# Kernel tuning notes

Measured on AMD Instinct MI355X. Metric: run time of the kernel, lower is better.

Reference implementation:

```python
import jax, jax.numpy as jnp
import numpy as np

DEFAULT_MASK_VALUE = -0.7 * float(jnp.finfo(jnp.dtype('float32')).max)

B, T, NQ, NKV, D = 2, 1024, 32, 8, 128


def setup_inputs() -> dict:
    key = jax.random.key(0)
    k1, k2, k3, k4 = jax.random.split(key, 4)
    query = jax.random.normal(k1, (B, T, NQ, D), dtype=jnp.float32)
    kk = jax.random.normal(k2, (B, T, NKV, D), dtype=jnp.float32)
    vv = jax.random.normal(k3, (B, T, NKV, D), dtype=jnp.float32)
    # packed-sequence segment ids, sorted so each segment is contiguous (values 1..3, >0 = active)
    decoder_segment_ids = jnp.sort(jax.random.randint(k4, (B, T), 1, 4), axis=-1).astype(jnp.int32)
    return {"query": query, "key": kk, "value": vv,
            "decoder_segment_ids": decoder_segment_ids}


def _attention(query, key, value, decoder_segment_ids):
    # MaxText AttentionOp.apply_attention_dot (prefill / train mode), GQA layout.
    b, t, n, d = query.shape
    n_kv = key.shape[2]
    g = n // n_kv
    q = query.reshape(b, t, n_kv, g, d)
    # qk product: [b, n_kv, g, t, s]
    logits = jnp.einsum('btkgd,bskd->bkgts', q, key)
    # generate_attention_mask: segment mask AND causal mask
    seg_mask = decoder_segment_ids[:, :, None] == decoder_segment_ids[:, None, :]  # [b,t,s]
    row_ids = jax.lax.broadcasted_iota(jnp.int32, (t, t), 0)
    col_ids = jax.lax.broadcasted_iota(jnp.int32, (t, t), 1)
    causal = col_ids <= row_ids  # [t,s]
    mask = jnp.logical_and(seg_mask, causal[None])  # [b,t,s]
    # apply_mask_to_logits: replace masked entries with DEFAULT_MASK_VALUE (avoids add fusion)
    masked = jnp.where(mask[:, None, None, :, :], logits, DEFAULT_MASK_VALUE)
    probs = jax.nn.softmax(masked, axis=-1)
    out = jnp.einsum('bkgts,bskd->btkgd', probs, value)
    return out.reshape(b, t, n, d)


def reference(query, key, value, decoder_segment_ids):
    return _attention(query, key, value, decoder_segment_ids)
```

## Files before the change

### kernel.cpp

```cpp
#include <hip/hip_runtime.h>

constexpr int B_  = 2;
constexpr int T_  = 1024;
constexpr int NQ  = 32;
constexpr int NKV = 8;
constexpr int D_  = 128;

constexpr int BM = 64;
constexpr int BN = 32;
constexpr int NTILE = T_ / BM;
constexpr float MASK_NEG = -3.0e38f;

typedef _Float16 f16;
typedef f16 f16x2 __attribute__((ext_vector_type(2)));
typedef f16 f16x4 __attribute__((ext_vector_type(4)));
typedef f16 f16x8 __attribute__((ext_vector_type(8)));
typedef float floatx4 __attribute__((ext_vector_type(4)));

__global__ __launch_bounds__(256)
void fa_kernel(const float* __restrict__ Qg, const float* __restrict__ Kg,
               const float* __restrict__ Vg, const int* __restrict__ seg,
               float* __restrict__ Og) {
    __shared__ f16 lds_k[BN][136];
    __shared__ f16 lds_vt[D_][40];
    __shared__ f16 lds_p[4][16][40];

    const int pair = blockIdx.x;
    const int h    = blockIdx.y;
    const int b    = blockIdx.z;
    const int kv   = h >> 2;

    const int tid  = threadIdx.x;
    const int wave = tid >> 6;
    const int lane = tid & 63;
    const int quad = lane >> 4;
    const int ln   = lane & 15;

    const int kd4 = tid & 31, kr8 = tid >> 5;
    const int vd  = tid & 127, vhalf = tid >> 7;

    const int* segb = seg + b * T_;

    for (int sub = 0; sub < 2; ++sub) {
        const int tile = (sub == 0) ? (NTILE - 1 - pair) : pair;
        const int t0 = tile * BM;

        const int qrow = t0 + wave * 16 + ln;
        const float* qptr = Qg + (((size_t)b * T_ + qrow) * NQ + h) * D_;
        f16x8 qfrag[4];
#pragma unroll
        for (int c = 0; c < 4; ++c) {
            const float* p = qptr + c * 32 + quad * 8;
            float4 f0 = *(const float4*)(p);
            float4 f1 = *(const float4*)(p + 4);
            f16x8 v;
            v[0] = (f16)f0.x; v[1] = (f16)f0.y; v[2] = (f16)f0.z; v[3] = (f16)f0.w;
            v[4] = (f16)f1.x; v[5] = (f16)f1.y; v[6] = (f16)f1.z; v[7] = (f16)f1.w;
            qfrag[c] = v;
        }

        int trow[4], segq[4];
#pragma unroll
        for (int r = 0; r < 4; ++r) {
            trow[r] = t0 + wave * 16 + quad * 4 + r;
            segq[r] = segb[trow[r]];
        }
        const int seg_lo = segb[t0];

        int lo = 0, hi = t0;
        while (lo < hi) {
            const int mid = (lo + hi) >> 1;
            if (segb[mid] < seg_lo) lo = mid + 1; else hi = mid;
        }
        const int blk_start = lo >> 5;
        const int nblk = 2 * tile + 2;

        float  m_i[4], l_i[4];
        floatx4 o_acc[8];
#pragma unroll
        for (int r = 0; r < 4; ++r) { m_i[r] = -1.0e30f; l_i[r] = 0.0f; }
#pragma unroll
        for (int dt = 0; dt < 8; ++dt) o_acc[dt] = floatx4{0.f, 0.f, 0.f, 0.f};

        float4 kreg[4];
        float  vreg[16];
        {
            const int s0 = blk_start * BN;
            const float* kb = Kg + (((size_t)b * T_ + s0 + kr8) * NKV + kv) * D_ + kd4 * 4;
#pragma unroll
            for (int i = 0; i < 4; ++i)
                kreg[i] = *(const float4*)(kb + (size_t)(8 * i) * NKV * D_);
            const float* vb = Vg + (((size_t)b * T_ + s0 + vhalf * 16) * NKV + kv) * D_ + vd;
#pragma unroll
            for (int i = 0; i < 16; ++i)
                vreg[i] = vb[(size_t)i * NKV * D_];
        }

        for (int blk = blk_start; blk < nblk; ++blk) {
            const int s0 = blk * BN;
            __syncthreads();

#pragma unroll
            for (int i = 0; i < 4; ++i) {
                f16x4 w;
                w[0] = (f16)kreg[i].x; w[1] = (f16)kreg[i].y;
                w[2] = (f16)kreg[i].z; w[3] = (f16)kreg[i].w;
                *(f16x4*)&lds_k[kr8 + 8 * i][kd4 * 4] = w;
            }
#pragma unroll
            for (int i = 0; i < 8; ++i) {
                f16x2 w; w[0] = (f16)vreg[2 * i]; w[1] = (f16)vreg[2 * i + 1];
                *(f16x2*)&lds_vt[vd][vhalf * 16 + 2 * i] = w;
            }

            if (blk + 1 < nblk) {
                const int s0n = s0 + BN;
                const float* kb = Kg + (((size_t)b * T_ + s0n + kr8) * NKV + kv) * D_ + kd4 * 4;
#pragma unroll
                for (int i = 0; i < 4; ++i)
                    kreg[i] = *(const float4*)(kb + (size_t)(8 * i) * NKV * D_);
                const float* vb = Vg + (((size_t)b * T_ + s0n + vhalf * 16) * NKV + kv) * D_ + vd;
#pragma unroll
                for (int i = 0; i < 16; ++i)
                    vreg[i] = vb[(size_t)i * NKV * D_];
            }
            __syncthreads();

            floatx4 sc[2];
#pragma unroll
            for (int nt = 0; nt < 2; ++nt) {
                floatx4 acc = floatx4{0.f, 0.f, 0.f, 0.f};
#pragma unroll
                for (int c = 0; c < 4; ++c) {
                    f16x8 kf = *(const f16x8*)&lds_k[nt * 16 + ln][c * 32 + quad * 8];
                    acc = __builtin_amdgcn_mfma_f32_16x16x32_f16(qfrag[c], kf, acc, 0, 0, 0);
                }
                sc[nt] = acc;
            }

            int segs[2];
            segs[0] = segb[s0 + ln];
            segs[1] = segb[s0 + 16 + ln];
#pragma unroll
            for (int nt = 0; nt < 2; ++nt) {
                const int s = s0 + nt * 16 + ln;
#pragma unroll
                for (int r = 0; r < 4; ++r) {
                    const bool ok = (s <= trow[r]) && (segs[nt] == segq[r]);
                    sc[nt][r] = ok ? sc[nt][r] : MASK_NEG;
                }
            }

            float pr[2][4];
#pragma unroll
            for (int r = 0; r < 4; ++r) {
                float mx = fmaxf(sc[0][r], sc[1][r]);
                mx = fmaxf(mx, __shfl_xor(mx, 1));
                mx = fmaxf(mx, __shfl_xor(mx, 2));
                mx = fmaxf(mx, __shfl_xor(mx, 4));
                mx = fmaxf(mx, __shfl_xor(mx, 8));
                const float mnew  = fmaxf(m_i[r], mx);
                const float alpha = __expf(m_i[r] - mnew);
                m_i[r] = mnew;
                const float p0 = __expf(sc[0][r] - mnew);
                const float p1 = __expf(sc[1][r] - mnew);
                pr[0][r] = p0; pr[1][r] = p1;
                float sm = p0 + p1;
                sm += __shfl_xor(sm, 1);
                sm += __shfl_xor(sm, 2);
                sm += __shfl_xor(sm, 4);
                sm += __shfl_xor(sm, 8);
                l_i[r] = l_i[r] * alpha + sm;
#pragma unroll
                for (int dt = 0; dt < 8; ++dt) o_acc[dt][r] *= alpha;
            }

#pragma unroll
            for (int nt = 0; nt < 2; ++nt)
#pragma unroll
                for (int r = 0; r < 4; ++r)
                    lds_p[wave][quad * 4 + r][nt * 16 + ln] = (f16)pr[nt][r];

            __threadfence_block();

            f16x8 afrag = *(const f16x8*)&lds_p[wave][ln][quad * 8];
#pragma unroll
            for (int dt = 0; dt < 8; ++dt) {
                f16x8 bfrag = *(const f16x8*)&lds_vt[dt * 16 + ln][quad * 8];
                o_acc[dt] = __builtin_amdgcn_mfma_f32_16x16x32_f16(afrag, bfrag, o_acc[dt], 0, 0, 0);
            }
        }

#pragma unroll
        for (int r = 0; r < 4; ++r) {
            const float inv = 1.0f / l_i[r];
            float* optr = Og + (((size_t)b * T_ + trow[r]) * NQ + h) * D_ + ln;
#pragma unroll
            for (int dt = 0; dt < 8; ++dt)
                optr[dt * 16] = o_acc[dt][r] * inv;
        }
    }
}

extern "C" void kernel_launch(void* const* d_in, const int* in_sizes, int n_in,
                              void* d_out, int out_size, void* d_ws, size_t ws_size,
                              hipStream_t stream) {
    const float* Q   = (const float*)d_in[0];
    const float* K   = (const float*)d_in[1];
    const float* V   = (const float*)d_in[2];
    const int*   seg = (const int*)d_in[3];
    float* out = (float*)d_out;
    dim3 grid(NTILE / 2, NQ, B_);
    fa_kernel<<<grid, 256, 0, stream>>>(Q, K, V, seg, out);
}
```

Before: 141.4 us.

## Widen KV tile to 64, cache segment ids in LDS, ballot block start

```diff
diff --git a/kernel.cpp b/kernel.cpp
--- a/kernel.cpp
+++ b/kernel.cpp
@@ -7,7 +7,7 @@
 constexpr int D_  = 128;
 
 constexpr int BM = 64;
-constexpr int BN = 32;
+constexpr int BN = 64;
 constexpr int NTILE = T_ / BM;
 constexpr float MASK_NEG = -3.0e38f;
 
@@ -22,8 +22,9 @@
                const float* __restrict__ Vg, const int* __restrict__ seg,
                float* __restrict__ Og) {
     __shared__ f16 lds_k[BN][136];
-    __shared__ f16 lds_vt[D_][40];
-    __shared__ f16 lds_p[4][16][40];
+    __shared__ f16 lds_vt[D_][72];
+    __shared__ f16 lds_p[4][16][72];
+    __shared__ int lds_seg[T_];
 
     const int pair = blockIdx.x;
     const int h    = blockIdx.y;
@@ -40,9 +41,11 @@
     const int vd  = tid & 127, vhalf = tid >> 7;
 
     const int* segb = seg + b * T_;
+    *(int4*)&lds_seg[tid * 4] = *(const int4*)(segb + tid * 4);
+    __syncthreads();
 
     for (int sub = 0; sub < 2; ++sub) {
-        const int tile = (sub == 0) ? (NTILE - 1 - pair) : pair;
+        const int tile = sub ? pair : (NTILE - 1 - pair);
         const int t0 = tile * BM;
 
         const int qrow = t0 + wave * 16 + ln;
@@ -63,17 +66,13 @@
 #pragma unroll
         for (int r = 0; r < 4; ++r) {
             trow[r] = t0 + wave * 16 + quad * 4 + r;
-            segq[r] = segb[trow[r]];
-        }
-        const int seg_lo = segb[t0];
-
-        int lo = 0, hi = t0;
-        while (lo < hi) {
-            const int mid = (lo + hi) >> 1;
-            if (segb[mid] < seg_lo) lo = mid + 1; else hi = mid;
-        }
-        const int blk_start = lo >> 5;
-        const int nblk = 2 * tile + 2;
+            segq[r] = lds_seg[trow[r]];
+        }
+        const int seg_lo = lds_seg[t0];
+
+        unsigned long long bal = __ballot(lds_seg[lane * 16 + 15] < seg_lo);
+        const int blk_start = __popcll(bal) >> 2;
+        const int nblk = tile + 1;
 
         float  m_i[4], l_i[4];
         floatx4 o_acc[8];
@@ -82,17 +81,17 @@
 #pragma unroll
         for (int dt = 0; dt < 8; ++dt) o_acc[dt] = floatx4{0.f, 0.f, 0.f, 0.f};
 
-        float4 kreg[4];
-        float  vreg[16];
+        float4 kreg[8];
+        float  vreg[32];
         {
             const int s0 = blk_start * BN;
             const float* kb = Kg + (((size_t)b * T_ + s0 + kr8) * NKV + kv) * D_ + kd4 * 4;
 #pragma unroll
-            for (int i = 0; i < 4; ++i)
+            for (int i = 0; i < 8; ++i)
                 kreg[i] = *(const float4*)(kb + (size_t)(8 * i) * NKV * D_);
-            const float* vb = Vg + (((size_t)b * T_ + s0 + vhalf * 16) * NKV + kv) * D_ + vd;
-#pragma unroll
-            for (int i = 0; i < 16; ++i)
+            const float* vb = Vg + (((size_t)b * T_ + s0 + vhalf * 32) * NKV + kv) * D_ + vd;
+#pragma unroll
+            for (int i = 0; i < 32; ++i)
                 vreg[i] = vb[(size_t)i * NKV * D_];
         }
 
@@ -101,34 +100,34 @@
             __syncthreads();
 
 #pragma unroll
-            for (int i = 0; i < 4; ++i) {
+            for (int i = 0; i < 8; ++i) {
                 f16x4 w;
                 w[0] = (f16)kreg[i].x; w[1] = (f16)kreg[i].y;
                 w[2] = (f16)kreg[i].z; w[3] = (f16)kreg[i].w;
                 *(f16x4*)&lds_k[kr8 + 8 * i][kd4 * 4] = w;
             }
 #pragma unroll
-            for (int i = 0; i < 8; ++i) {
+            for (int i = 0; i < 16; ++i) {
                 f16x2 w; w[0] = (f16)vreg[2 * i]; w[1] = (f16)vreg[2 * i + 1];
-                *(f16x2*)&lds_vt[vd][vhalf * 16 + 2 * i] = w;
-            }
+                *(f16x2*)&lds_vt[vd][vhalf * 32 + 2 * i] = w;
+            }
+            __syncthreads();
 
             if (blk + 1 < nblk) {
                 const int s0n = s0 + BN;
                 const float* kb = Kg + (((size_t)b * T_ + s0n + kr8) * NKV + kv) * D_ + kd4 * 4;
 #pragma unroll
-                for (int i = 0; i < 4; ++i)
+                for (int i = 0; i < 8; ++i)
                     kreg[i] = *(const float4*)(kb + (size_t)(8 * i) * NKV * D_);
-                const float* vb = Vg + (((size_t)b * T_ + s0n + vhalf * 16) * NKV + kv) * D_ + vd;
-#pragma unroll
-                for (int i = 0; i < 16; ++i)
+                const float* vb = Vg + (((size_t)b * T_ + s0n + vhalf * 32) * NKV + kv) * D_ + vd;
+#pragma unroll
+                for (int i = 0; i < 32; ++i)
                     vreg[i] = vb[(size_t)i * NKV * D_];
             }
-            __syncthreads();
-
-            floatx4 sc[2];
-#pragma unroll
-            for (int nt = 0; nt < 2; ++nt) {
+
+            floatx4 sc[4];
+#pragma unroll
+            for (int nt = 0; nt < 4; ++nt) {
                 floatx4 acc = floatx4{0.f, 0.f, 0.f, 0.f};
 #pragma unroll
                 for (int c = 0; c < 4; ++c) {
@@ -138,23 +137,20 @@
                 sc[nt] = acc;
             }
 
-            int segs[2];
-            segs[0] = segb[s0 + ln];
-            segs[1] = segb[s0 + 16 + ln];
-#pragma unroll
-            for (int nt = 0; nt < 2; ++nt) {
+#pragma unroll
+            for (int nt = 0; nt < 4; ++nt) {
                 const int s = s0 + nt * 16 + ln;
+                const int sgs = lds_seg[s];
 #pragma unroll
                 for (int r = 0; r < 4; ++r) {
-                    const bool ok = (s <= trow[r]) && (segs[nt] == segq[r]);
+                    const bool ok = (s <= trow[r]) && (sgs == segq[r]);
                     sc[nt][r] = ok ? sc[nt][r] : MASK_NEG;
                 }
             }
 
-            float pr[2][4];
 #pragma unroll
             for (int r = 0; r < 4; ++r) {
-                float mx = fmaxf(sc[0][r], sc[1][r]);
+                float mx = fmaxf(fmaxf(sc[0][r], sc[1][r]), fmaxf(sc[2][r], sc[3][r]));
                 mx = fmaxf(mx, __shfl_xor(mx, 1));
                 mx = fmaxf(mx, __shfl_xor(mx, 2));
                 mx = fmaxf(mx, __shfl_xor(mx, 4));
@@ -162,10 +158,12 @@
                 const float mnew  = fmaxf(m_i[r], mx);
                 const float alpha = __expf(m_i[r] - mnew);
                 m_i[r] = mnew;
-                const float p0 = __expf(sc[0][r] - mnew);
-                const float p1 = __expf(sc[1][r] - mnew);
-                pr[0][r] = p0; pr[1][r] = p1;
-                float sm = p0 + p1;
+                float p0 = __expf(sc[0][r] - mnew);
+                float p1 = __expf(sc[1][r] - mnew);
+                float p2 = __expf(sc[2][r] - mnew);
+                float p3 = __expf(sc[3][r] - mnew);
+                sc[0][r] = p0; sc[1][r] = p1; sc[2][r] = p2; sc[3][r] = p3;
+                float sm = (p0 + p1) + (p2 + p3);
                 sm += __shfl_xor(sm, 1);
                 sm += __shfl_xor(sm, 2);
                 sm += __shfl_xor(sm, 4);
@@ -176,18 +174,22 @@
             }
 
 #pragma unroll
-            for (int nt = 0; nt < 2; ++nt)
+            for (int nt = 0; nt < 4; ++nt)
 #pragma unroll
                 for (int r = 0; r < 4; ++r)
-                    lds_p[wave][quad * 4 + r][nt * 16 + ln] = (f16)pr[nt][r];
-
-            __threadfence_block();
-
-            f16x8 afrag = *(const f16x8*)&lds_p[wave][ln][quad * 8];
+                    lds_p[wave][quad * 4 + r][nt * 16 + ln] = (f16)sc[nt][r];
+
+            __builtin_amdgcn_s_waitcnt(0xc07f);
+
+            f16x8 af0 = *(const f16x8*)&lds_p[wave][ln][quad * 8];
+            f16x8 af1 = *(const f16x8*)&lds_p[wave][ln][32 + quad * 8];
+
 #pragma unroll
             for (int dt = 0; dt < 8; ++dt) {
-                f16x8 bfrag = *(const f16x8*)&lds_vt[dt * 16 + ln][quad * 8];
-                o_acc[dt] = __builtin_amdgcn_mfma_f32_16x16x32_f16(afrag, bfrag, o_acc[dt], 0, 0, 0);
+                f16x8 b0 = *(const f16x8*)&lds_vt[dt * 16 + ln][quad * 8];
+                f16x8 b1 = *(const f16x8*)&lds_vt[dt * 16 + ln][32 + quad * 8];
+                o_acc[dt] = __builtin_amdgcn_mfma_f32_16x16x32_f16(af0, b0, o_acc[dt], 0, 0, 0);
+                o_acc[dt] = __builtin_amdgcn_mfma_f32_16x16x32_f16(af1, b1, o_acc[dt], 0, 0, 0);
             }
         }
 
```

Measured after the change: 131.0 us. 1.08x faster.
